# Kernel optimization log

Measured on AMD Instinct MI355X. Metric: run time of the kernel, lower is better.

## Reference

```python
import jax, jax.numpy as jnp
import numpy as np

N_NODES = 2_000_000
E = 1_000_000
MEM = 32      # memory_dim
MSG = 32      # message_dim
EMB = 32      # embed_dim
EDGE = 2      # edge_dim


def _linear_params(key, out_dim, in_dim):
    kw, kb = jax.random.split(key)
    bound = 1.0 / np.sqrt(in_dim)
    W = jax.random.uniform(kw, (out_dim, in_dim), jnp.float32, -bound, bound)
    b = jax.random.uniform(kb, (out_dim,), jnp.float32, -bound, bound)
    return W, b


def setup_inputs() -> dict:
    key = jax.random.key(0)
    ks = jax.random.split(key, 16)
    inp = {}
    inp["src_ids"] = jax.random.randint(ks[0], (E,), 0, N_NODES)
    inp["dst_ids"] = jax.random.randint(ks[1], (E,), 0, N_NODES)
    inp["edge_feat"] = jax.random.normal(ks[2], (E, EDGE), jnp.float32)
    inp["delta_t"] = jax.random.uniform(ks[3], (E, 1), jnp.float32)
    # persistent node memory (torch init is zeros; use randn for a non-trivial baseline)
    inp["memory"] = jax.random.normal(ks[4], (N_NODES, MEM), jnp.float32) * 0.1
    # MessageFunction MLP: (2*MEM + EDGE + 1) -> MSG -> MSG
    inp["msg_W1"], inp["msg_b1"] = _linear_params(ks[5], MSG, 2 * MEM + EDGE + 1)
    inp["msg_W2"], inp["msg_b2"] = _linear_params(ks[6], MSG, MSG)
    # GRUCell(MSG, MEM): weight_ih [3*MEM, MSG], weight_hh [3*MEM, MEM]
    inp["gru_w_ih"], inp["gru_b_ih"] = _linear_params(ks[7], 3 * MEM, MSG)
    inp["gru_w_hh"], inp["gru_b_hh"] = _linear_params(ks[8], 3 * MEM, MEM)
    # MultiheadAttention with seq_len=1: only V and out projections affect output
    inp["attn_Wv"], inp["attn_bv"] = _linear_params(ks[9], MEM, MEM)
    inp["attn_Wo"], inp["attn_bo"] = _linear_params(ks[10], MEM, MEM)
    # TemporalEmbedding MLP: (MEM + EDGE) -> EMB -> EMB
    inp["emb_W1"], inp["emb_b1"] = _linear_params(ks[11], EMB, MEM + EDGE)
    inp["emb_W2"], inp["emb_b2"] = _linear_params(ks[12], EMB, EMB)
    # AnomalyClassifier: EMB -> 32 -> 1
    inp["cls_W1"], inp["cls_b1"] = _linear_params(ks[13], 32, EMB)
    inp["cls_W2"], inp["cls_b2"] = _linear_params(ks[14], 1, 32)
    return inp


def reference(src_ids, dst_ids, edge_feat, delta_t, memory,
              msg_W1, msg_b1, msg_W2, msg_b2,
              gru_w_ih, gru_w_hh, gru_b_ih, gru_b_hh,
              attn_Wv, attn_bv, attn_Wo, attn_bo,
              emb_W1, emb_b1, emb_W2, emb_b2,
              cls_W1, cls_b1, cls_W2, cls_b2):
    # gather per-node memory  [E, MEM]
    src_mem = memory[src_ids]
    dst_mem = memory[dst_ids]

    # MessageFunction: concat + 2-layer MLP
    x = jnp.concatenate([src_mem, dst_mem, edge_feat, delta_t], axis=-1)  # [E, 67]
    h = jax.nn.relu(x @ msg_W1.T + msg_b1)
    msg = h @ msg_W2.T + msg_b2  # [E, MSG]

    # GRUCell update on dst memory (torch gate order: r, z, n)
    gi = msg @ gru_w_ih.T + gru_b_ih      # [E, 3*MEM]
    gh = dst_mem @ gru_w_hh.T + gru_b_hh  # [E, 3*MEM]
    i_r, i_z, i_n = jnp.split(gi, 3, axis=-1)
    h_r, h_z, h_n = jnp.split(gh, 3, axis=-1)
    r = jax.nn.sigmoid(i_r + h_r)
    z = jax.nn.sigmoid(i_z + h_z)
    n = jnp.tanh(i_n + r * h_n)
    updated = (1.0 - z) * n + z * dst_mem  # [E, MEM]
    # scatter back into persistent buffer (detached in the torch module)
    new_memory = memory.at[dst_ids].set(jax.lax.stop_gradient(updated))

    # TemporalEmbedding: self-attention over a length-1 sequence. softmax of a
    # single score is exactly 1, so attn_out == out_proj(v_proj(dst_mem)).
    attn_out = (dst_mem @ attn_Wv.T + attn_bv) @ attn_Wo.T + attn_bo  # [E, MEM]
    e = jnp.concatenate([attn_out, edge_feat], axis=-1)  # [E, MEM+EDGE]
    embed = jax.nn.relu(e @ emb_W1.T + emb_b1) @ emb_W2.T + emb_b2  # [E, EMB]

    # AnomalyClassifier (dropout is identity at eval)
    logits = jax.nn.relu(embed @ cls_W1.T + cls_b1) @ cls_W2.T + cls_b2  # [E, 1]
    probs = jax.nn.sigmoid(logits).squeeze(-1)  # [E]
    return probs, new_memory
```

## Files before the change

kernel.cpp:

```cpp
#include <hip/hip_runtime.h>
#include <hip/hip_bf16.h>

typedef float  f32x4v __attribute__((ext_vector_type(4)));
typedef short  bf16x8 __attribute__((ext_vector_type(8)));

#define NFRAG   26
#define TB_F32  512
#define FRG_U16 (NFRAG*512)
#define SHARE_BYTES (TB_F32*4 + FRG_U16*2)
#define SHARE_U4 (SHARE_BYTES/16)
#define XPK_STRIDE 20
#define SM_F32 (SHARE_BYTES/4 + 4*16*XPK_STRIDE)
#define WC_OFF 7168

#define BLK 256
#define COPY_BLOCKS 256
#define EDGE_BLOCKS 768
#define GRID (COPY_BLOCKS + EDGE_BLOCKS)
#define EDGE_WAVES (EDGE_BLOCKS * 4)

#define MFMA(a,b,c) __builtin_amdgcn_mfma_f32_16x16x32_bf16(a,b,c,0,0,0)

__device__ __forceinline__ float sigf(float v) { return 1.0f / (1.0f + __expf(-v)); }
__device__ __forceinline__ float tanhf_fast(float v) {
    float a = fabsf(v);
    float t = __expf(-2.0f * a);
    float r = (1.0f - t) / (1.0f + t);
    return v < 0.0f ? -r : r;
}
__device__ __forceinline__ unsigned pk(float a, float b) {
    union { __hip_bfloat162 h; unsigned u; } c;
    c.h = __float22bfloat162_rn(make_float2(a, b));
    return c.u;
}

union FragU { uint4 u4; bf16x8 s8; unsigned u[4]; };

__device__ __forceinline__ bf16x8 ldfrag(const unsigned short* frg, int idx_u16) {
    FragU c; c.u4 = *(const uint4*)(frg + idx_u16); return c.s8;
}
__device__ __forceinline__ f32x4v tbl(const float* tb, int idx_f32) {
    return *(const f32x4v*)(tb + idx_f32);
}
__device__ __forceinline__ bf16x8 relayout(f32x4v h0, f32x4v h1, unsigned* xw, int eI, int g) {
    *(uint2*)(xw + eI * XPK_STRIDE + 2 * g)     = make_uint2(pk(h0[0], h0[1]), pk(h0[2], h0[3]));
    *(uint2*)(xw + eI * XPK_STRIDE + 8 + 2 * g) = make_uint2(pk(h1[0], h1[1]), pk(h1[2], h1[3]));
    FragU c; c.u4 = *(const uint4*)(xw + eI * XPK_STRIDE + 4 * g);
    return c.s8;
}

__global__ void winner_k(const int* __restrict__ dst_ids, int* __restrict__ winner, int E) {
    int e = blockIdx.x * 256 + threadIdx.x;
    if (e < E) atomicMax(winner + dst_ids[e], e + 1);
}

__global__ void prep_k(const float* __restrict__ msg_W1, const float* __restrict__ msg_b1,
                       const float* __restrict__ msg_W2, const float* __restrict__ msg_b2,
                       const float* __restrict__ w_ih, const float* __restrict__ b_ih,
                       const float* __restrict__ w_hh, const float* __restrict__ b_hh,
                       const float* __restrict__ Wv, const float* __restrict__ bv,
                       const float* __restrict__ Wo, const float* __restrict__ bo,
                       const float* __restrict__ emb_W1, const float* __restrict__ emb_b1,
                       const float* __restrict__ emb_W2, const float* __restrict__ emb_b2,
                       const float* __restrict__ cls_W1, const float* __restrict__ cls_b1,
                       const float* __restrict__ cls_W2, float* __restrict__ WSf) {
    int t = threadIdx.x;
    float* tb = WSf;
    unsigned short* frg = (unsigned short*)(WSf + TB_F32);
    float* WC = WSf + WC_OFF;
    if (t < 32) {
        int j = t;
        tb[0*32+j]  = msg_b1[j];
        tb[1*32+j]  = msg_W1[j*67+64];
        tb[2*32+j]  = msg_W1[j*67+65];
        tb[3*32+j]  = msg_W1[j*67+66];
        tb[4*32+j]  = msg_b2[j];
        tb[5*32+j]  = b_ih[32+j] + b_hh[32+j];
        tb[6*32+j]  = b_ih[j] + b_hh[j];
        tb[7*32+j]  = b_hh[64+j];
        tb[8*32+j]  = b_ih[64+j];
        float a = bo[j];
        for (int o = 0; o < 32; ++o) a += Wo[j*32+o] * bv[o];
        tb[9*32+j]  = a;
        tb[10*32+j] = emb_b1[j];
        tb[11*32+j] = emb_W1[j*34+32];
        tb[12*32+j] = emb_W1[j*34+33];
        tb[13*32+j] = emb_b2[j];
        tb[14*32+j] = cls_b1[j];
        tb[15*32+j] = cls_W2[j];
    }
    for (int i = t; i < 1024; i += 256) {
        int j = i >> 5, k = i & 31;
        float a = 0.0f;
        for (int o = 0; o < 32; ++o) a += Wo[j*32+o] * Wv[o*32+k];
        WC[i] = a;
    }
    __syncthreads();
    for (int idx = t; idx < NFRAG * 512; idx += 256) {
        int f = idx >> 9, l = (idx >> 3) & 63, i = idx & 7;
        int r = l & 15, kb = ((l >> 4) << 3) + i;
        const float* P; int j0 = 0, k0 = 0, ld = 32;
        switch (f) {
            case 0:  P = msg_W1; j0 = 0;  k0 = 0;  ld = 67; break;
            case 1:  P = msg_W1; j0 = 0;  k0 = 32; ld = 67; break;
            case 2:  P = msg_W1; j0 = 16; k0 = 0;  ld = 67; break;
            case 3:  P = msg_W1; j0 = 16; k0 = 32; ld = 67; break;
            case 4:  P = msg_W2; j0 = 0;  break;
            case 5:  P = msg_W2; j0 = 16; break;
            case 6:  P = w_ih;   j0 = 32; break;
            case 7:  P = w_hh;   j0 = 32; break;
            case 8:  P = w_ih;   j0 = 48; break;
            case 9:  P = w_hh;   j0 = 48; break;
            case 10: P = w_ih;   j0 = 0;  break;
            case 11: P = w_hh;   j0 = 0;  break;
            case 12: P = w_ih;   j0 = 16; break;
            case 13: P = w_hh;   j0 = 16; break;
            case 14: P = w_hh;   j0 = 64; break;
            case 15: P = w_hh;   j0 = 80; break;
            case 16: P = w_ih;   j0 = 64; break;
            case 17: P = w_ih;   j0 = 80; break;
            case 18: P = WC;     j0 = 0;  break;
            case 19: P = WC;     j0 = 16; break;
            case 20: P = emb_W1; j0 = 0;  ld = 34; break;
            case 21: P = emb_W1; j0 = 16; ld = 34; break;
            case 22: P = emb_W2; j0 = 0;  break;
            case 23: P = emb_W2; j0 = 16; break;
            case 24: P = cls_W1; j0 = 0;  break;
            default: P = cls_W1; j0 = 16; break;
        }
        __hip_bfloat16 hv = __float2bfloat16(P[(j0 + r) * ld + k0 + kb]);
        frg[idx] = *(unsigned short*)&hv;
    }
}

__device__ __forceinline__ void compute16(
    int grp, int E, int eI, int g, int lane,
    int e, int dst, int winv, float2 ef, float dtv,
    f32x4v sa, f32x4v sb, f32x4v da, f32x4v db, f32x4v t0, f32x4v t1,
    const float* tb, const unsigned short* frg, unsigned* xw, float clsb2,
    float* __restrict__ probs, float* __restrict__ out_mem) {
    int ob = 0, tbo = 0;
    asm volatile("" : "+v"(ob), "+v"(tbo));

    FragU Bs, Bd;
    Bs.u[0] = pk(sa[0], sa[1]); Bs.u[1] = pk(sa[2], sa[3]);
    Bs.u[2] = pk(sb[0], sb[1]); Bs.u[3] = pk(sb[2], sb[3]);
    Bd.u[0] = pk(da[0], da[1]); Bd.u[1] = pk(da[2], da[3]);
    Bd.u[2] = pk(db[0], db[1]); Bd.u[3] = pk(db[2], db[3]);
    f32x4v dmt[2]; dmt[0] = t0; dmt[1] = t1;

    f32x4v h[2];
#pragma unroll
    for (int jt = 0; jt < 2; ++jt) {
        f32x4v b1v = tbl(tb, 0*32 + jt*16 + 4*g + tbo);
        f32x4v w64 = tbl(tb, 1*32 + jt*16 + 4*g + tbo);
        f32x4v w65 = tbl(tb, 2*32 + jt*16 + 4*g + tbo);
        f32x4v w66 = tbl(tb, 3*32 + jt*16 + 4*g + tbo);
        f32x4v c;
#pragma unroll
        for (int i = 0; i < 4; ++i)
            c[i] = b1v[i] + ef.x * w64[i] + ef.y * w65[i] + dtv * w66[i];
        c = MFMA(ldfrag(frg, (jt*2+1)*512 + lane*8 + ob), Bd.s8, c);
        c = MFMA(ldfrag(frg, (jt*2+0)*512 + lane*8 + ob), Bs.s8, c);
#pragma unroll
        for (int i = 0; i < 4; ++i) c[i] = fmaxf(c[i], 0.0f);
        h[jt] = c;
    }
    bf16x8 Bh = relayout(h[0], h[1], xw, eI, g);

    f32x4v m[2];
#pragma unroll
    for (int jt = 0; jt < 2; ++jt)
        m[jt] = MFMA(ldfrag(frg, (4+jt)*512 + lane*8 + ob), Bh,
                     tbl(tb, 4*32 + jt*16 + 4*g + tbo));
    bf16x8 Bm = relayout(m[0], m[1], xw, eI, g);

    f32x4v zz[2], uu[2];
#pragma unroll
    for (int jt = 0; jt < 2; ++jt) {
        f32x4v c = tbl(tb, 5*32 + jt*16 + 4*g + tbo);
        c = MFMA(ldfrag(frg, (7+2*jt)*512 + lane*8 + ob), Bd.s8, c);
        c = MFMA(ldfrag(frg, (6+2*jt)*512 + lane*8 + ob), Bm, c);
#pragma unroll
        for (int i = 0; i < 4; ++i) c[i] = sigf(c[i]);
        zz[jt] = c;
    }
#pragma unroll
    for (int jt = 0; jt < 2; ++jt) {
        f32x4v c = tbl(tb, 6*32 + jt*16 + 4*g + tbo);
        c = MFMA(ldfrag(frg, (11+2*jt)*512 + lane*8 + ob), Bd.s8, c);
        c = MFMA(ldfrag(frg, (10+2*jt)*512 + lane*8 + ob), Bm, c);
        f32x4v hn = tbl(tb, 7*32 + jt*16 + 4*g + tbo);
        hn = MFMA(ldfrag(frg, (14+jt)*512 + lane*8 + ob), Bd.s8, hn);
        f32x4v bin = tbl(tb, 8*32 + jt*16 + 4*g + tbo);
        f32x4v npre;
#pragma unroll
        for (int i = 0; i < 4; ++i) npre[i] = fmaf(sigf(c[i]), hn[i], bin[i]);
        npre = MFMA(ldfrag(frg, (16+jt)*512 + lane*8 + ob), Bm, npre);
#pragma unroll
        for (int i = 0; i < 4; ++i) {
            float n = tanhf_fast(npre[i]);
            uu[jt][i] = n + zz[jt][i] * (dmt[jt][i] - n);
        }
    }
    if (winv == e + 1) {
        f32x4v* orow = (f32x4v*)(out_mem + (size_t)dst * 32);
        orow[g]     = uu[0];
        orow[4 + g] = uu[1];
    }

    f32x4v at[2];
#pragma unroll
    for (int jt = 0; jt < 2; ++jt)
        at[jt] = MFMA(ldfrag(frg, (18+jt)*512 + lane*8 + ob), Bd.s8,
                      tbl(tb, 9*32 + jt*16 + 4*g + tbo));
    bf16x8 Ba = relayout(at[0], at[1], xw, eI, g);
    f32x4v e1v[2];
#pragma unroll
    for (int jt = 0; jt < 2; ++jt) {
        f32x4v b  = tbl(tb, 10*32 + jt*16 + 4*g + tbo);
        f32x4v wa = tbl(tb, 11*32 + jt*16 + 4*g + tbo);
        f32x4v wb = tbl(tb, 12*32 + jt*16 + 4*g + tbo);
        f32x4v c;
#pragma unroll
        for (int i = 0; i < 4; ++i) c[i] = b[i] + ef.x * wa[i] + ef.y * wb[i];
        c = MFMA(ldfrag(frg, (20+jt)*512 + lane*8 + ob), Ba, c);
#pragma unroll
        for (int i = 0; i < 4; ++i) c[i] = fmaxf(c[i], 0.0f);
        e1v[jt] = c;
    }
    bf16x8 B1 = relayout(e1v[0], e1v[1], xw, eI, g);
    f32x4v e2v[2];
#pragma unroll
    for (int jt = 0; jt < 2; ++jt)
        e2v[jt] = MFMA(ldfrag(frg, (22+jt)*512 + lane*8 + ob), B1,
                       tbl(tb, 13*32 + jt*16 + 4*g + tbo));
    bf16x8 B2 = relayout(e2v[0], e2v[1], xw, eI, g);
    float part = 0.0f;
#pragma unroll
    for (int jt = 0; jt < 2; ++jt) {
        f32x4v c = MFMA(ldfrag(frg, (24+jt)*512 + lane*8 + ob), B2,
                        tbl(tb, 14*32 + jt*16 + 4*g + tbo));
        f32x4v w2 = tbl(tb, 15*32 + jt*16 + 4*g + tbo);
#pragma unroll
        for (int i = 0; i < 4; ++i) part = fmaf(fmaxf(c[i], 0.0f), w2[i], part);
    }
    part += __shfl_xor(part, 16);
    part += __shfl_xor(part, 32);
    if (lane < 16) {
        int ee = grp * 16 + eI;
        if (ee < E) probs[ee] = sigf(part + clsb2);
    }
}

__global__ __launch_bounds__(BLK, 4) void tgn_mfma16(
    const int* __restrict__ src_ids, const int* __restrict__ dst_ids,
    const float* __restrict__ edge_feat, const float* __restrict__ delta_t,
    const float* __restrict__ memory, const float* __restrict__ cls_b2,
    const float* __restrict__ WSf, const int* __restrict__ winner,
    float* __restrict__ probs, float* __restrict__ out_mem,
    int E, int N, int ngrp) {
    __shared__ float smem[SM_F32];
    int bid = blockIdx.x, tid = threadIdx.x;

    if (bid < COPY_BLOCKS) {
        const f32x4v* m4 = (const f32x4v*)memory;
        f32x4v* o4 = (f32x4v*)out_mem;
        const long S = (long)COPY_BLOCKS * BLK;
        const long total4 = (long)N * 8;
        long i0 = (long)bid * BLK + tid;
        for (; i0 + 3 * S < total4; i0 += 4 * S) {
            long i1 = i0 + S, i2 = i0 + 2 * S, i3 = i0 + 3 * S;
            int w0 = winner[i0 >> 3];
            int w1 = winner[i1 >> 3];
            int w2 = winner[i2 >> 3];
            int w3 = winner[i3 >> 3];
            if (w0 == 0) o4[i0] = m4[i0];
            if (w1 == 0) o4[i1] = m4[i1];
            if (w2 == 0) o4[i2] = m4[i2];
            if (w3 == 0) o4[i3] = m4[i3];
        }
        for (; i0 < total4; i0 += S) {
            if (winner[i0 >> 3] == 0) o4[i0] = m4[i0];
        }
        return;
    }

    {
        const uint4* s = (const uint4*)WSf;
        uint4* d = (uint4*)smem;
        for (int i = tid; i < SHARE_U4; i += BLK) d[i] = s[i];
    }
    __syncthreads();
    const float* tb = smem;
    const unsigned short* frg = (const unsigned short*)(smem + TB_F32);
    int wv = tid >> 6, lane = tid & 63;
    int eI = lane & 15, g = lane >> 4;
    unsigned* xw = (unsigned*)(smem + SHARE_BYTES / 4) + wv * (16 * XPK_STRIDE);
    int ewid = (bid - COPY_BLOCKS) * 4 + wv;
    float clsb2 = cls_b2[0];

#define PREF(P, G) do {                                                              \
    int ee = (G) * 16 + eI; if (ee >= E) ee = E - 1;                                 \
    e##P = ee;                                                                       \
    int sid = src_ids[ee]; dst##P = dst_ids[ee];                                     \
    ef##P = ((const float2*)edge_feat)[ee]; dt##P = delta_t[ee];                     \
    win##P = winner[dst##P];                                                         \
    const f32x4v* sp_ = (const f32x4v*)(memory + (size_t)sid * 32);                  \
    const f32x4v* dp_ = (const f32x4v*)(memory + (size_t)dst##P * 32);               \
    S##P##a = sp_[2*g]; S##P##b = sp_[2*g+1];                                        \
    D##P##a = dp_[2*g]; D##P##b = dp_[2*g+1];                                        \
    T##P##0 = dp_[g];   T##P##1 = dp_[4+g];                                          \
} while (0)

    int g0 = ewid;
    if (g0 < ngrp) {
        int eA, dstA, winA; float2 efA; float dtA;
        f32x4v SAa, SAb, DAa, DAb, TA0, TA1;
        int eB, dstB, winB; float2 efB; float dtB;
        f32x4v SBa, SBb, DBa, DBb, TB0, TB1;
        PREF(A, g0);
        for (;;) {
            int gn = g0 + EDGE_WAVES;
            { int gp = (gn < ngrp) ? gn : (ngrp - 1); PREF(B, gp); }
            asm volatile("" ::: "memory");
            compute16(g0, E, eI, g, lane, eA, dstA, winA, efA, dtA,
                      SAa, SAb, DAa, DAb, TA0, TA1,
                      tb, frg, xw, clsb2, probs, out_mem);
            if (gn >= ngrp) break;
            g0 = gn;
            gn = g0 + EDGE_WAVES;
            { int gp = (gn < ngrp) ? gn : (ngrp - 1); PREF(A, gp); }
            asm volatile("" ::: "memory");
            compute16(g0, E, eI, g, lane, eB, dstB, winB, efB, dtB,
                      SBa, SBb, DBa, DBb, TB0, TB1,
                      tb, frg, xw, clsb2, probs, out_mem);
            if (gn >= ngrp) break;
            g0 = gn;
        }
    }
#undef PREF
}

extern "C" void kernel_launch(void* const* d_in, const int* in_sizes, int n_in,
                              void* d_out, int out_size, void* d_ws, size_t ws_size,
                              hipStream_t stream) {
    const int*   src_ids   = (const int*)d_in[0];
    const int*   dst_ids   = (const int*)d_in[1];
    const float* edge_feat = (const float*)d_in[2];
    const float* delta_t   = (const float*)d_in[3];
    const float* memory    = (const float*)d_in[4];
    const float* msg_W1 = (const float*)d_in[5],  *msg_b1 = (const float*)d_in[6];
    const float* msg_W2 = (const float*)d_in[7],  *msg_b2 = (const float*)d_in[8];
    const float* w_ih   = (const float*)d_in[9],  *b_ih   = (const float*)d_in[10];
    const float* w_hh   = (const float*)d_in[11], *b_hh   = (const float*)d_in[12];
    const float* Wv     = (const float*)d_in[13], *bv     = (const float*)d_in[14];
    const float* Wo     = (const float*)d_in[15], *bo     = (const float*)d_in[16];
    const float* emb_W1 = (const float*)d_in[17], *emb_b1 = (const float*)d_in[18];
    const float* emb_W2 = (const float*)d_in[19], *emb_b2 = (const float*)d_in[20];
    const float* cls_W1 = (const float*)d_in[21], *cls_b1 = (const float*)d_in[22];
    const float* cls_W2 = (const float*)d_in[23], *cls_b2 = (const float*)d_in[24];

    int E = in_sizes[0];
    int N = in_sizes[4] / 32;
    int ngrp = (E + 15) / 16;

    int*   winner = (int*)d_ws;
    float* WSf    = (float*)((char*)d_ws + (size_t)N * sizeof(int));
    float* probs  = (float*)d_out;
    float* outmem = probs + E;

    hipMemsetAsync(winner, 0, (size_t)N * sizeof(int), stream);
    winner_k<<<(E + 255) / 256, 256, 0, stream>>>(dst_ids, winner, E);
    prep_k<<<1, 256, 0, stream>>>(msg_W1, msg_b1, msg_W2, msg_b2,
                                  w_ih, b_ih, w_hh, b_hh,
                                  Wv, bv, Wo, bo,
                                  emb_W1, emb_b1, emb_W2, emb_b2,
                                  cls_W1, cls_b1, cls_W2, WSf);
    tgn_mfma16<<<GRID, BLK, 0, stream>>>(src_ids, dst_ids, edge_feat, delta_t,
                                         memory, cls_b2, WSf, winner,
                                         probs, outmem, E, N, ngrp);
}
```

Before: 293.5 us.

## Permute weight K-layout so MFMA outputs feed next layer from registers

Replaces the LDS round-trip relayout between chained MFMA layers with an in-register bf16 pack. To make this valid, the prep kernel permutes the K index of the weight fragments that consume those activations, matching the accumulator layout. Dropping the per-wave scratch LDS lowers shared memory use, so edge blocks rise from 768 to 1024 and launch bounds go to 5 blocks per CU. The risk is that a wrong permutation silently corrupts results, and the higher occupancy target may add register pressure.

```diff
diff --git a/kernel.cpp b/kernel.cpp
--- a/kernel.cpp
+++ b/kernel.cpp
@@ -9,13 +9,11 @@
 #define FRG_U16 (NFRAG*512)
 #define SHARE_BYTES (TB_F32*4 + FRG_U16*2)
 #define SHARE_U4 (SHARE_BYTES/16)
-#define XPK_STRIDE 20
-#define SM_F32 (SHARE_BYTES/4 + 4*16*XPK_STRIDE)
 #define WC_OFF 7168
 
 #define BLK 256
 #define COPY_BLOCKS 256
-#define EDGE_BLOCKS 768
+#define EDGE_BLOCKS 1024
 #define GRID (COPY_BLOCKS + EDGE_BLOCKS)
 #define EDGE_WAVES (EDGE_BLOCKS * 4)
 
@@ -42,10 +40,10 @@
 __device__ __forceinline__ f32x4v tbl(const float* tb, int idx_f32) {
     return *(const f32x4v*)(tb + idx_f32);
 }
-__device__ __forceinline__ bf16x8 relayout(f32x4v h0, f32x4v h1, unsigned* xw, int eI, int g) {
-    *(uint2*)(xw + eI * XPK_STRIDE + 2 * g)     = make_uint2(pk(h0[0], h0[1]), pk(h0[2], h0[3]));
-    *(uint2*)(xw + eI * XPK_STRIDE + 8 + 2 * g) = make_uint2(pk(h1[0], h1[1]), pk(h1[2], h1[3]));
-    FragU c; c.u4 = *(const uint4*)(xw + eI * XPK_STRIDE + 4 * g);
+__device__ __forceinline__ bf16x8 relayout_reg(f32x4v h0, f32x4v h1) {
+    FragU c;
+    c.u[0] = pk(h0[0], h0[1]); c.u[1] = pk(h0[2], h0[3]);
+    c.u[2] = pk(h1[0], h1[1]); c.u[3] = pk(h1[2], h1[3]);
     return c.s8;
 }
 
@@ -100,35 +98,38 @@
         int f = idx >> 9, l = (idx >> 3) & 63, i = idx & 7;
         int r = l & 15, kb = ((l >> 4) << 3) + i;
         const float* P; int j0 = 0, k0 = 0, ld = 32;
+        bool mapped = false;
         switch (f) {
             case 0:  P = msg_W1; j0 = 0;  k0 = 0;  ld = 67; break;
             case 1:  P = msg_W1; j0 = 0;  k0 = 32; ld = 67; break;
             case 2:  P = msg_W1; j0 = 16; k0 = 0;  ld = 67; break;
             case 3:  P = msg_W1; j0 = 16; k0 = 32; ld = 67; break;
-            case 4:  P = msg_W2; j0 = 0;  break;
-            case 5:  P = msg_W2; j0 = 16; break;
-            case 6:  P = w_ih;   j0 = 32; break;
+            case 4:  P = msg_W2; j0 = 0;  mapped = true; break;
+            case 5:  P = msg_W2; j0 = 16; mapped = true; break;
+            case 6:  P = w_ih;   j0 = 32; mapped = true; break;
             case 7:  P = w_hh;   j0 = 32; break;
-            case 8:  P = w_ih;   j0 = 48; break;
+            case 8:  P = w_ih;   j0 = 48; mapped = true; break;
             case 9:  P = w_hh;   j0 = 48; break;
-            case 10: P = w_ih;   j0 = 0;  break;
+            case 10: P = w_ih;   j0 = 0;  mapped = true; break;
             case 11: P = w_hh;   j0 = 0;  break;
-            case 12: P = w_ih;   j0 = 16; break;
+            case 12: P = w_ih;   j0 = 16; mapped = true; break;
             case 13: P = w_hh;   j0 = 16; break;
             case 14: P = w_hh;   j0 = 64; break;
             case 15: P = w_hh;   j0 = 80; break;
-            case 16: P = w_ih;   j0 = 64; break;
-            case 17: P = w_ih;   j0 = 80; break;
+            case 16: P = w_ih;   j0 = 64; mapped = true; break;
+            case 17: P = w_ih;   j0 = 80; mapped = true; break;
             case 18: P = WC;     j0 = 0;  break;
             case 19: P = WC;     j0 = 16; break;
-            case 20: P = emb_W1; j0 = 0;  ld = 34; break;
-            case 21: P = emb_W1; j0 = 16; ld = 34; break;
-            case 22: P = emb_W2; j0 = 0;  break;
-            case 23: P = emb_W2; j0 = 16; break;
-            case 24: P = cls_W1; j0 = 0;  break;
-            default: P = cls_W1; j0 = 16; break;
-        }
-        __hip_bfloat16 hv = __float2bfloat16(P[(j0 + r) * ld + k0 + kb]);
+            case 20: P = emb_W1; j0 = 0;  ld = 34; mapped = true; break;
+            case 21: P = emb_W1; j0 = 16; ld = 34; mapped = true; break;
+            case 22: P = emb_W2; j0 = 0;  mapped = true; break;
+            case 23: P = emb_W2; j0 = 16; mapped = true; break;
+            case 24: P = cls_W1; j0 = 0;  mapped = true; break;
+            default: P = cls_W1; j0 = 16; mapped = true; break;
+        }
+        int kidx = kb;
+        if (mapped) kidx = 16 * ((kb >> 2) & 1) + 4 * (kb >> 3) + (kb & 3);
+        __hip_bfloat16 hv = __float2bfloat16(P[(j0 + r) * ld + k0 + kidx]);
         frg[idx] = *(unsigned short*)&hv;
     }
 }
@@ -137,7 +138,7 @@
     int grp, int E, int eI, int g, int lane,
     int e, int dst, int winv, float2 ef, float dtv,
     f32x4v sa, f32x4v sb, f32x4v da, f32x4v db, f32x4v t0, f32x4v t1,
-    const float* tb, const unsigned short* frg, unsigned* xw, float clsb2,
+    const float* tb, const unsigned short* frg, float clsb2,
     float* __restrict__ probs, float* __restrict__ out_mem) {
     int ob = 0, tbo = 0;
     asm volatile("" : "+v"(ob), "+v"(tbo));
@@ -166,14 +167,14 @@
         for (int i = 0; i < 4; ++i) c[i] = fmaxf(c[i], 0.0f);
         h[jt] = c;
     }
-    bf16x8 Bh = relayout(h[0], h[1], xw, eI, g);
+    bf16x8 Bh = relayout_reg(h[0], h[1]);
 
     f32x4v m[2];
 #pragma unroll
     for (int jt = 0; jt < 2; ++jt)
         m[jt] = MFMA(ldfrag(frg, (4+jt)*512 + lane*8 + ob), Bh,
                      tbl(tb, 4*32 + jt*16 + 4*g + tbo));
-    bf16x8 Bm = relayout(m[0], m[1], xw, eI, g);
+    bf16x8 Bm = relayout_reg(m[0], m[1]);
 
     f32x4v zz[2], uu[2];
 #pragma unroll
@@ -214,7 +215,7 @@
     for (int jt = 0; jt < 2; ++jt)
         at[jt] = MFMA(ldfrag(frg, (18+jt)*512 + lane*8 + ob), Bd.s8,
                       tbl(tb, 9*32 + jt*16 + 4*g + tbo));
-    bf16x8 Ba = relayout(at[0], at[1], xw, eI, g);
+    bf16x8 Ba = relayout_reg(at[0], at[1]);
     f32x4v e1v[2];
 #pragma unroll
     for (int jt = 0; jt < 2; ++jt) {
@@ -229,13 +230,13 @@
         for (int i = 0; i < 4; ++i) c[i] = fmaxf(c[i], 0.0f);
         e1v[jt] = c;
     }
-    bf16x8 B1 = relayout(e1v[0], e1v[1], xw, eI, g);
+    bf16x8 B1 = relayout_reg(e1v[0], e1v[1]);
     f32x4v e2v[2];
 #pragma unroll
     for (int jt = 0; jt < 2; ++jt)
         e2v[jt] = MFMA(ldfrag(frg, (22+jt)*512 + lane*8 + ob), B1,
                        tbl(tb, 13*32 + jt*16 + 4*g + tbo));
-    bf16x8 B2 = relayout(e2v[0], e2v[1], xw, eI, g);
+    bf16x8 B2 = relayout_reg(e2v[0], e2v[1]);
     float part = 0.0f;
 #pragma unroll
     for (int jt = 0; jt < 2; ++jt) {
@@ -253,14 +254,14 @@
     }
 }
 
-__global__ __launch_bounds__(BLK, 4) void tgn_mfma16(
+__global__ __launch_bounds__(BLK, 5) void tgn_mfma16(
     const int* __restrict__ src_ids, const int* __restrict__ dst_ids,
     const float* __restrict__ edge_feat, const float* __restrict__ delta_t,
     const float* __restrict__ memory, const float* __restrict__ cls_b2,
     const float* __restrict__ WSf, const int* __restrict__ winner,
     float* __restrict__ probs, float* __restrict__ out_mem,
     int E, int N, int ngrp) {
-    __shared__ float smem[SM_F32];
+    __shared__ uint4 sbuf[SHARE_U4];
     int bid = blockIdx.x, tid = threadIdx.x;
 
     if (bid < COPY_BLOCKS) {
@@ -288,15 +289,13 @@
 
     {
         const uint4* s = (const uint4*)WSf;
-        uint4* d = (uint4*)smem;
-        for (int i = tid; i < SHARE_U4; i += BLK) d[i] = s[i];
+        for (int i = tid; i < SHARE_U4; i += BLK) sbuf[i] = s[i];
     }
     __syncthreads();
-    const float* tb = smem;
-    const unsigned short* frg = (const unsigned short*)(smem + TB_F32);
+    const float* tb = (const float*)sbuf;
+    const unsigned short* frg = (const unsigned short*)((const float*)sbuf + TB_F32);
     int wv = tid >> 6, lane = tid & 63;
     int eI = lane & 15, g = lane >> 4;
-    unsigned* xw = (unsigned*)(smem + SHARE_BYTES / 4) + wv * (16 * XPK_STRIDE);
     int ewid = (bid - COPY_BLOCKS) * 4 + wv;
     float clsb2 = cls_b2[0];
 
@@ -326,7 +325,7 @@
             asm volatile("" ::: "memory");
             compute16(g0, E, eI, g, lane, eA, dstA, winA, efA, dtA,
                       SAa, SAb, DAa, DAb, TA0, TA1,
-                      tb, frg, xw, clsb2, probs, out_mem);
+                      tb, frg, clsb2, probs, out_mem);
             if (gn >= ngrp) break;
             g0 = gn;
             gn = g0 + EDGE_WAVES;
@@ -334,7 +333,7 @@
             asm volatile("" ::: "memory");
             compute16(g0, E, eI, g, lane, eB, dstB, winB, efB, dtB,
                       SBa, SBb, DBa, DBb, TB0, TB1,
-                      tb, frg, xw, clsb2, probs, out_mem);
+                      tb, frg, clsb2, probs, out_mem);
             if (gn >= ngrp) break;
             g0 = gn;
         }
```

Measured after the change: 298.8 us. No clear change (+1.8%).
